# Optimization experiments

Measured on AMD Instinct MI355X. Metric: run time of the kernel, lower is better.

## Reference

```python
import jax, jax.numpy as jnp
import numpy as np

L, B, T, C, H, FF = 2, 2, 2048, 512, 8, 1024
HS = C // H  # head size
EPS = 1.1920929e-07  # torch float32 finfo eps (nn.RMSNorm default)


def setup_inputs() -> dict:
    key = jax.random.key(0)
    ks = jax.random.split(key, 20)
    s = 0.02
    return {
        "hidden": jax.random.normal(ks[0], (B, T, C), jnp.float32),
        "target": jax.random.normal(ks[1], (B, T, C), jnp.float32),
        # self-attn per-head projections (bias=False)
        "Wq_s": jax.random.normal(ks[2], (L, H, C, HS)) * s,
        "Wk_s": jax.random.normal(ks[3], (L, H, C, HS)) * s,
        "Wv_s": jax.random.normal(ks[4], (L, H, C, HS)) * s,
        "Wo_s": jax.random.normal(ks[5], (L, C, C)) * s,
        "bo_s": jnp.zeros((L, C)),
        # cross-attn per-head projections
        "Wq_x": jax.random.normal(ks[6], (L, H, C, HS)) * s,
        "Wk_x": jax.random.normal(ks[7], (L, H, C, HS)) * s,
        "Wv_x": jax.random.normal(ks[8], (L, H, C, HS)) * s,
        "Wo_x": jax.random.normal(ks[9], (L, C, C)) * s,
        "bo_x": jnp.zeros((L, C)),
        # FFN
        "W1": jax.random.normal(ks[10], (L, C, FF)) * s,
        "b1": jnp.zeros((L, FF)),
        "W2": jax.random.normal(ks[11], (L, FF, C)) * s,
        "b2": jnp.zeros((L, C)),
        # RMSNorm gains ln1..ln4
        "g1": jnp.ones((L, C)),
        "g2": jnp.ones((L, C)),
        "g3": jnp.ones((L, C)),
        "g4": jnp.ones((L, C)),
    }


def _rms(x, g):
    return x * jax.lax.rsqrt(jnp.mean(x * x, axis=-1, keepdims=True) + EPS) * g


def _attn(q_in, kv_in, Wq, Wk, Wv, Wo, bo, causal):
    # q_in: [B,Tq,C], kv_in: [B,Tk,C]; W*: [H,C,HS]
    q = jnp.einsum('btc,hcd->bhtd', q_in, Wq)
    k = jnp.einsum('bsc,hcd->bhsd', kv_in, Wk)
    v = jnp.einsum('bsc,hcd->bhsd', kv_in, Wv)
    wei = jnp.einsum('bhtd,bhsd->bhts', q, k) * (HS ** -0.5)  # [B,H,Tq,Tk]
    if causal:
        Tq, Tk = q_in.shape[1], kv_in.shape[1]
        mask = jnp.tril(jnp.ones((Tq, Tk), bool))
        wei = jnp.where(mask, wei, -jnp.inf)
    wei = jax.nn.softmax(wei, axis=-1)
    out = jnp.einsum('bhts,bhsd->bhtd', wei, v)
    out = out.transpose(0, 2, 1, 3).reshape(q_in.shape[0], q_in.shape[1], C)
    return out @ Wo + bo


def reference(hidden, target, Wq_s, Wk_s, Wv_s, Wo_s, bo_s,
              Wq_x, Wk_x, Wv_x, Wo_x, bo_x,
              W1, b1, W2, b2, g1, g2, g3, g4):
    t = target
    for l in range(L):
        # masked self-attention with RMSNorm pre-norm + residual
        t = t + _attn(_rms(t, g1[l]), _rms(t, g1[l]), Wq_s[l], Wk_s[l], Wv_s[l],
                      Wo_s[l], bo_s[l], causal=True)
        # cross-attention: K/V from ln2(hidden), Q from ln3(t)
        t = t + _attn(_rms(t, g3[l]), _rms(hidden, g2[l]), Wq_x[l], Wk_x[l], Wv_x[l],
                      Wo_x[l], bo_x[l], causal=False)
        # GELU FFN
        h = _rms(t, g4[l])
        t = t + (jax.nn.gelu(h @ W1[l] + b1[l], approximate=False) @ W2[l] + b2[l])
    return t
```

## Files before the change

kernel.cpp:

```cpp
#include <hip/hip_runtime.h>
#include <hip/hip_bf16.h>
#include <math.h>

#define L 2
#define B 2
#define T 2048
#define C 512
#define H 8
#define FF 1024
#define HS 64
#define EPSV 1.1920929e-07f

typedef __hip_bfloat16 bf16;
typedef __attribute__((ext_vector_type(8))) short short8;
typedef __attribute__((ext_vector_type(4))) float f32x4;

__device__ __forceinline__ float b2f(bf16 x) { return __bfloat162float(x); }

__device__ __forceinline__ void gl16(const unsigned short* g, unsigned short* l) {
    __builtin_amdgcn_global_load_lds(
        (const __attribute__((address_space(1))) unsigned int*)g,
        (__attribute__((address_space(3))) unsigned int*)l, 16, 0, 0);
}

__global__ void detect_k(const unsigned short* __restrict__ g1bits, int* __restrict__ flag) {
    if (threadIdx.x == 0 && blockIdx.x == 0)
        *flag = (g1bits[0] != (unsigned short)0x3F80u) ? 1 : 0;
}

__device__ __forceinline__ float ld_in(const void* p, size_t i, int fl) {
    return fl ? ((const float*)p)[i] : b2f(((const bf16*)p)[i]);
}

#define QKVT_TOT 1572864
#define WO_TOT 524288
#define W12_TOT 1048576
#define SM_TOT 9216
#define ACT_TOT 2097152
#define PREP_TOT (2 * QKVT_TOT + 2 * WO_TOT + 2 * W12_TOT + SM_TOT + 2 * ACT_TOT)

struct PrepArgs {
    const void *Wq_s, *Wk_s, *Wv_s, *Wo_s, *Wq_x, *Wk_x, *Wv_x, *Wo_x, *W1, *W2;
    const void* sm[8];
    const void *hidden, *target;
    bf16 *cQKVs, *cQKVx, *cWoTs, *cWoTx, *cW1T, *cW2T, *smallDst;
    float *hid, *t_buf;
    const int* flag;
};

__global__ void prep_k(PrepArgs pa) {
    long long i = (long long)blockIdx.x * 256 + threadIdx.x;
    if (i >= PREP_TOT) return;
    int fl = *pa.flag;
    if (i < 2LL * QKVT_TOT) {
        int which = i >= QKVT_TOT;
        int j = (int)(i - (long long)which * QKVT_TOT);
        int l = j / 786432, r = j - l * 786432;
        int n = r >> 9, c = r & 511;
        int p = n >> 9, nn = n & 511;
        int hh = nn >> 6, d = nn & 63;
        const void* src = which ? (p == 0 ? pa.Wq_x : p == 1 ? pa.Wk_x : pa.Wv_x)
                                : (p == 0 ? pa.Wq_s : p == 1 ? pa.Wk_s : pa.Wv_s);
        size_t si = ((size_t)(l * 8 + hh) * 512 + c) * 64 + d;
        (which ? pa.cQKVx : pa.cQKVs)[j] = __float2bfloat16(ld_in(src, si, fl));
        return;
    }
    i -= 2LL * QKVT_TOT;
    if (i < 2LL * WO_TOT) {
        int which = i >= WO_TOT;
        int j = (int)(i - (long long)which * WO_TOT);
        int l = j >> 18, r = j & 262143;
        int n = r >> 9, c = r & 511;
        size_t si = ((size_t)l << 18) + ((size_t)c << 9) + n;
        (which ? pa.cWoTx : pa.cWoTs)[j] = __float2bfloat16(ld_in(which ? pa.Wo_x : pa.Wo_s, si, fl));
        return;
    }
    i -= 2LL * WO_TOT;
    if (i < W12_TOT) {
        int j = (int)i;
        int l = j >> 19, r = j & 524287;
        int n = r >> 9, c = r & 511;
        size_t si = ((size_t)l << 19) + ((size_t)c << 10) + n;
        pa.cW1T[j] = __float2bfloat16(ld_in(pa.W1, si, fl));
        return;
    }
    i -= W12_TOT;
    if (i < W12_TOT) {
        int j = (int)i;
        int l = j >> 19, r = j & 524287;
        int n = r >> 10, c = r & 1023;
        size_t si = ((size_t)l << 19) + ((size_t)c << 9) + n;
        pa.cW2T[j] = __float2bfloat16(ld_in(pa.W2, si, fl));
        return;
    }
    i -= W12_TOT;
    if (i < SM_TOT) {
        int j = (int)i;
        const int cum[9] = {0, 1024, 2048, 4096, 5120, 6144, 7168, 8192, 9216};
        int k = 0;
        while (j >= cum[k + 1]) k++;
        pa.smallDst[j] = __float2bfloat16(ld_in(pa.sm[k], j - cum[k], fl));
        return;
    }
    i -= SM_TOT;
    if (i < ACT_TOT) {
        pa.hid[i] = ld_in(pa.hidden, (size_t)i, fl);
    } else {
        size_t j = i - ACT_TOT;
        pa.t_buf[j] = ld_in(pa.target, j, fl);
    }
}

__global__ void write_out_k(const float* __restrict__ in, void* __restrict__ out, int n,
                            const int* __restrict__ flag) {
    int i = blockIdx.x * blockDim.x + threadIdx.x;
    if (i >= n) return;
    if (*flag) ((float*)out)[i] = in[i];
    else       ((bf16*)out)[i] = __float2bfloat16(in[i]);
}

__global__ void rmsnorm_k(const float* __restrict__ x, const bf16* __restrict__ g,
                          bf16* __restrict__ y) {
    int row = blockIdx.x;
    int tid = threadIdx.x;
    const float* xr = x + (size_t)row * C;
    float v0 = xr[tid], v1 = xr[tid + 256];
    __shared__ float red[256];
    red[tid] = v0 * v0 + v1 * v1;
    __syncthreads();
    for (int s = 128; s > 0; s >>= 1) {
        if (tid < s) red[tid] += red[tid + s];
        __syncthreads();
    }
    float sc = rsqrtf(red[0] / (float)C + EPSV);
    y[(size_t)row * C + tid] = __float2bfloat16(v0 * sc * b2f(g[tid]));
    y[(size_t)row * C + tid + 256] = __float2bfloat16(v1 * sc * b2f(g[tid + 256]));
}

__global__ void rmsnorm2_k(const float* __restrict__ xa, const bf16* __restrict__ ga,
                           bf16* __restrict__ ya, const float* __restrict__ xb,
                           const bf16* __restrict__ gb, bf16* __restrict__ yb) {
    int sel = blockIdx.y;
    const float* x = sel ? xb : xa;
    const bf16* g = sel ? gb : ga;
    bf16* y = sel ? yb : ya;
    int row = blockIdx.x;
    int tid = threadIdx.x;
    const float* xr = x + (size_t)row * C;
    float v0 = xr[tid], v1 = xr[tid + 256];
    __shared__ float red[256];
    red[tid] = v0 * v0 + v1 * v1;
    __syncthreads();
    for (int s = 128; s > 0; s >>= 1) {
        if (tid < s) red[tid] += red[tid + s];
        __syncthreads();
    }
    float sc = rsqrtf(red[0] / (float)C + EPSV);
    y[(size_t)row * C + tid] = __float2bfloat16(v0 * sc * b2f(g[tid]));
    y[(size_t)row * C + tid + 256] = __float2bfloat16(v1 * sc * b2f(g[tid + 256]));
}

struct GDesc {
    const bf16* A; const bf16* Bt; const bf16* bias; float* resid; bf16* out;
    int N, K, ldOut, ep, nblkx, blkofs;
};
struct GBatch { GDesc d[3]; int nd; };

__global__ __launch_bounds__(256) void gemm64_k(GBatch gb) {
    int bid = blockIdx.x;
    int di = 0;
    if (gb.nd > 1 && bid >= gb.d[1].blkofs) di = 1;
    if (gb.nd > 2 && bid >= gb.d[2].blkofs) di = 2;
    GDesc g = gb.d[di];
    int lb = bid - g.blkofs;
    int bx = lb % g.nblkx, by = lb / g.nblkx;
    int m0 = by * 64, n0 = bx * 64;

    __shared__ alignas(16) unsigned short As[2][64 * 64];
    __shared__ alignas(16) unsigned short Bs[2][64 * 64];
    int tid = threadIdx.x, lane = tid & 63, wave = tid >> 6;
    int wr = wave >> 1, wc = wave & 1, quad = lane >> 4, l15 = lane & 15;
    const unsigned short* Au = (const unsigned short*)g.A;
    const unsigned short* Bu = (const unsigned short*)g.Bt;

    int r0 = tid >> 3, sg = tid & 7;
    int gs = sg ^ (r0 & 7);
    const unsigned short* agp0 = Au + (size_t)(m0 + r0) * g.K + gs * 8;
    const unsigned short* agp1 = Au + (size_t)(m0 + r0 + 32) * g.K + gs * 8;
    const unsigned short* bgp0 = Bu + (size_t)(n0 + r0) * g.K + gs * 8;
    const unsigned short* bgp1 = Bu + (size_t)(n0 + r0 + 32) * g.K + gs * 8;
    int wofs = wave * 512;

    f32x4 zf = {0.f, 0.f, 0.f, 0.f};
    f32x4 acc[2][2];
    acc[0][0] = zf; acc[0][1] = zf; acc[1][0] = zf; acc[1][1] = zf;

    int sws0 = ((quad) ^ (l15 & 7)) * 8;
    int sws1 = ((4 + quad) ^ (l15 & 7)) * 8;
    int arow = wr * 32 + l15, brow = wc * 32 + l15;

    int nk = g.K >> 6;
    {
        gl16(agp0, &As[0][wofs]);
        gl16(agp1, &As[0][wofs + 2048]);
        gl16(bgp0, &Bs[0][wofs]);
        gl16(bgp1, &Bs[0][wofs + 2048]);
    }
    __syncthreads();
    int buf = 0;
    for (int kt = 0; kt < nk; kt++) {
        if (kt + 1 < nk) {
            int ko = (kt + 1) << 6;
            gl16(agp0 + ko, &As[buf ^ 1][wofs]);
            gl16(agp1 + ko, &As[buf ^ 1][wofs + 2048]);
            gl16(bgp0 + ko, &Bs[buf ^ 1][wofs]);
            gl16(bgp1 + ko, &Bs[buf ^ 1][wofs + 2048]);
        }
        const unsigned short* Ab = As[buf];
        const unsigned short* Bb = Bs[buf];
        short8 a0[2], b0[2], a1[2], b1[2];
#pragma unroll
        for (int i = 0; i < 2; i++) {
            int ra = (arow + i * 16) << 6, rb = (brow + i * 16) << 6;
            a0[i] = *(const short8*)(Ab + ra + sws0);
            a1[i] = *(const short8*)(Ab + ra + sws1);
            b0[i] = *(const short8*)(Bb + rb + sws0);
            b1[i] = *(const short8*)(Bb + rb + sws1);
        }
#pragma unroll
        for (int mi = 0; mi < 2; mi++)
#pragma unroll
            for (int ni = 0; ni < 2; ni++) {
                acc[mi][ni] =
                    __builtin_amdgcn_mfma_f32_16x16x32_bf16(a0[mi], b0[ni], acc[mi][ni], 0, 0, 0);
                acc[mi][ni] =
                    __builtin_amdgcn_mfma_f32_16x16x32_bf16(a1[mi], b1[ni], acc[mi][ni], 0, 0, 0);
            }
        __syncthreads();
        buf ^= 1;
    }

#pragma unroll
    for (int mi = 0; mi < 2; mi++) {
#pragma unroll
        for (int ni = 0; ni < 2; ni++) {
            int colg = n0 + wc * 32 + ni * 16 + l15;
            float bv = (g.ep == 1 || g.ep == 2) ? b2f(g.bias[colg]) : 0.f;
#pragma unroll
            for (int r2 = 0; r2 < 4; r2++) {
                int rowg = m0 + wr * 32 + mi * 16 + quad * 4 + r2;
                float v = acc[mi][ni][r2];
                if (g.ep == 0) {
                    g.out[(size_t)rowg * g.ldOut + colg] = __float2bfloat16(v);
                } else if (g.ep == 1) {
                    g.resid[(size_t)rowg * g.ldOut + colg] += v + bv;
                } else if (g.ep == 2) {
                    float u = v + bv;
                    g.out[(size_t)rowg * g.ldOut + colg] =
                        __float2bfloat16(0.5f * u * (1.f + erff(u * 0.70710678118654752f)));
                } else {
                    g.out[((size_t)((colg >> 11) * 512 + rowg) << 11) + (colg & 2047)] =
                        __float2bfloat16(v);
                }
            }
        }
    }
}

#define PST 72
__global__ __launch_bounds__(256) void attn_mfma_k(const bf16* __restrict__ qkv,
                                                   const bf16* __restrict__ vT,
                                                   bf16* __restrict__ attnout, int causal) {
    __shared__ unsigned short KsA[2][4096], VtA[2][4096];
    __shared__ unsigned short Ps[4][16 * PST];
    int qt = causal ? (gridDim.x - 1 - blockIdx.x) : blockIdx.x;
    int h = blockIdx.y, b = blockIdx.z;
    int tid = threadIdx.x, lane = tid & 63, w = tid >> 6;
    int quad = lane >> 4, l15 = lane & 15;
    const unsigned short* qk = (const unsigned short*)qkv;
    const unsigned short* vTp = (const unsigned short*)vT + ((size_t)b * 512 + h * 64) * T;
    size_t rowbase = (size_t)b * T;
    int koff = 512 + h * 64;
    unsigned short* Pw = Ps[w];
    bf16* Pwb = (bf16*)Pw;

    const unsigned short* qrow = qk + (rowbase + qt * 64 + w * 16 + l15) * 1536 + h * 64;
    short8 aq0 = *(const short8*)(qrow + quad * 8);
    short8 aq1 = *(const short8*)(qrow + 32 + quad * 8);

    int srow = lane >> 3;
    int ssp = (lane & 7) ^ (srow & 7);

    f32x4 zf = {0.f, 0.f, 0.f, 0.f};
    f32x4 oacc[4];
#pragma unroll
    for (int i = 0; i < 4; i++) oacc[i] = zf;
    float lpart[4] = {0.f, 0.f, 0.f, 0.f};

    int nT = causal ? (qt + 1) : (T / 64);

#pragma unroll
    for (int j = 0; j < 2; j++) {
        int c = w * 2 + j;
        int r = c * 8 + srow;
        gl16(qk + (rowbase + r) * 1536 + koff + ssp * 8, KsA[0] + c * 512);
        gl16(vTp + (size_t)r * T + ssp * 8, VtA[0] + c * 512);
    }
    __syncthreads();

    int buf = 0;
    for (int st = 0; st < nT; st++) {
        if (st + 1 < nT) {
#pragma unroll
            for (int j = 0; j < 2; j++) {
                int c = w * 2 + j;
                int r = c * 8 + srow;
                gl16(qk + (rowbase + (st + 1) * 64 + r) * 1536 + koff + ssp * 8,
                     KsA[buf ^ 1] + c * 512);
                gl16(vTp + (size_t)r * T + (st + 1) * 64 + ssp * 8, VtA[buf ^ 1] + c * 512);
            }
        }

        const unsigned short* Kb = KsA[buf];
        const unsigned short* Vb = VtA[buf];

        f32x4 sacc[4];
#pragma unroll
        for (int i = 0; i < 4; i++) sacc[i] = zf;
#pragma unroll
        for (int ni = 0; ni < 4; ni++) {
            int rr = ni * 16 + l15;
            short8 bk0 = *(const short8*)(Kb + rr * 64 + ((quad ^ (rr & 7)) * 8));
            short8 bk1 = *(const short8*)(Kb + rr * 64 + (((4 + quad) ^ (rr & 7)) * 8));
            sacc[ni] = __builtin_amdgcn_mfma_f32_16x16x32_bf16(aq0, bk0, sacc[ni], 0, 0, 0);
            sacc[ni] = __builtin_amdgcn_mfma_f32_16x16x32_bf16(aq1, bk1, sacc[ni], 0, 0, 0);
        }

        bool diag = causal && (st == qt);
        int qrl = w * 16 + quad * 4;
#pragma unroll
        for (int reg = 0; reg < 4; reg++) {
            float lp = 0.f;
#pragma unroll
            for (int ni = 0; ni < 4; ni++) {
                int s_l = ni * 16 + l15;
                float p = __expf(sacc[ni][reg] * 0.125f);
                if (diag && s_l > qrl + reg) p = 0.f;
                lp += p;
                Pwb[(quad * 4 + reg) * PST + s_l] = __float2bfloat16(p);
            }
            lpart[reg] += lp;
        }

        short8 ap0 = *(const short8*)(Pw + l15 * PST + quad * 8);
        short8 ap1 = *(const short8*)(Pw + l15 * PST + 32 + quad * 8);
#pragma unroll
        for (int dj = 0; dj < 4; dj++) {
            int rr = dj * 16 + l15;
            short8 bv0 = *(const short8*)(Vb + rr * 64 + ((quad ^ (rr & 7)) * 8));
            short8 bv1 = *(const short8*)(Vb + rr * 64 + (((4 + quad) ^ (rr & 7)) * 8));
            oacc[dj] = __builtin_amdgcn_mfma_f32_16x16x32_bf16(ap0, bv0, oacc[dj], 0, 0, 0);
            oacc[dj] = __builtin_amdgcn_mfma_f32_16x16x32_bf16(ap1, bv1, oacc[dj], 0, 0, 0);
        }

        __syncthreads();
        buf ^= 1;
    }

#pragma unroll
    for (int reg = 0; reg < 4; reg++) {
#pragma unroll
        for (int mk = 1; mk < 16; mk <<= 1) lpart[reg] += __shfl_xor(lpart[reg], mk, 64);
        lpart[reg] = 1.0f / lpart[reg];
    }
#pragma unroll
    for (int dj = 0; dj < 4; dj++) {
        int d = dj * 16 + l15;
#pragma unroll
        for (int reg = 0; reg < 4; reg++) {
            int q = w * 16 + quad * 4 + reg;
            attnout[(rowbase + qt * 64 + q) * C + h * HS + d] =
                __float2bfloat16(oacc[dj][reg] * lpart[reg]);
        }
    }
}

extern "C" void kernel_launch(void* const* d_in, const int* in_sizes, int n_in,
                              void* d_out, int out_size, void* d_ws, size_t ws_size,
                              hipStream_t stream) {
    const int BTC = B * T * C;
    const int BTF = B * T * FF;

    char* wsb = (char*)d_ws;
    int* flag = (int*)wsb;
    bf16* cur = (bf16*)(wsb + 256);
    bf16* cQKVs = cur;   cur += QKVT_TOT;
    bf16* cQKVx = cur;   cur += QKVT_TOT;
    bf16* cWoTs = cur;   cur += WO_TOT;
    bf16* cWoTx = cur;   cur += WO_TOT;
    bf16* cW1T = cur;    cur += W12_TOT;
    bf16* cW2T = cur;    cur += W12_TOT;
    bf16* smallBase = cur;
    bf16* cbo_s = cur;   cur += L * C;
    bf16* cbo_x = cur;   cur += L * C;
    bf16* cb1 = cur;     cur += L * FF;
    bf16* cb2 = cur;     cur += L * C;
    bf16* cg1 = cur;     cur += L * C;
    bf16* cg2 = cur;     cur += L * C;
    bf16* cg3 = cur;     cur += L * C;
    bf16* cg4 = cur;     cur += L * C;
    bf16* n1 = cur;      cur += BTC;
    bf16* n2 = cur;      cur += BTC;
    bf16* qkvbuf = cur;  cur += B * T * 3 * C;
    bf16* vTbuf = cur;   cur += BTC;
    bf16* attnout = cur; cur += BTC;
    bf16* h1buf = cur;   cur += BTF;
    size_t f32_off = (((char*)cur - wsb) + 255) & ~(size_t)255;
    float* t_buf = (float*)(wsb + f32_off);
    float* hid = t_buf + BTC;

    dim3 blk256(256);
    detect_k<<<1, 64, 0, stream>>>((const unsigned short*)d_in[16], flag);

    PrepArgs pa;
    pa.Wq_s = d_in[2]; pa.Wk_s = d_in[3]; pa.Wv_s = d_in[4]; pa.Wo_s = d_in[5];
    pa.Wq_x = d_in[7]; pa.Wk_x = d_in[8]; pa.Wv_x = d_in[9]; pa.Wo_x = d_in[10];
    pa.W1 = d_in[12]; pa.W2 = d_in[14];
    pa.sm[0] = d_in[6];  pa.sm[1] = d_in[11]; pa.sm[2] = d_in[13]; pa.sm[3] = d_in[15];
    pa.sm[4] = d_in[16]; pa.sm[5] = d_in[17]; pa.sm[6] = d_in[18]; pa.sm[7] = d_in[19];
    pa.hidden = d_in[0]; pa.target = d_in[1];
    pa.cQKVs = cQKVs; pa.cQKVx = cQKVx; pa.cWoTs = cWoTs; pa.cWoTx = cWoTx;
    pa.cW1T = cW1T; pa.cW2T = cW2T; pa.smallDst = smallBase;
    pa.hid = hid; pa.t_buf = t_buf; pa.flag = flag;
    prep_k<<<(PREP_TOT + 255) / 256, blk256, 0, stream>>>(pa);

    const int M = B * T;
    dim3 attngrid(T / 64, H, B);

    for (int l = 0; l < L; l++) {
        bf16* qkvW_s = cQKVs + (size_t)l * 3 * C * C;
        bf16* qkvW_x = cQKVx + (size_t)l * 3 * C * C;
        bf16* woT_s = cWoTs + (size_t)l * C * C;
        bf16* woT_x = cWoTx + (size_t)l * C * C;
        bf16* w1T = cW1T + (size_t)l * C * FF;
        bf16* w2T = cW2T + (size_t)l * FF * C;

        rmsnorm_k<<<M, blk256, 0, stream>>>(t_buf, cg1 + l * C, n1);
        {
            GBatch gb;
            gb.nd = 2;
            gb.d[0] = {n1, qkvW_s, nullptr, nullptr, qkvbuf, 1024, C, 3 * C, 0, 16, 0};
            gb.d[1] = {qkvW_s + (size_t)1024 * C, n1, nullptr, nullptr, vTbuf,
                       M, C, 0, 3, 64, 1024};
            gemm64_k<<<1024 + 512, blk256, 0, stream>>>(gb);
        }
        attn_mfma_k<<<attngrid, blk256, 0, stream>>>(qkvbuf, vTbuf, attnout, 1);
        {
            GBatch gb;
            gb.nd = 1;
            gb.d[0] = {attnout, woT_s, cbo_s + l * C, t_buf, nullptr, C, C, C, 1, 8, 0};
            gemm64_k<<<512, blk256, 0, stream>>>(gb);
        }

        rmsnorm2_k<<<dim3(M, 2), blk256, 0, stream>>>(t_buf, cg3 + l * C, n1, hid, cg2 + l * C, n2);
        {
            GBatch gb;
            gb.nd = 3;
            gb.d[0] = {n1, qkvW_x, nullptr, nullptr, qkvbuf, C, C, 3 * C, 0, 8, 0};
            gb.d[1] = {n2, qkvW_x + (size_t)512 * C, nullptr, nullptr, qkvbuf + C,
                       C, C, 3 * C, 0, 8, 512};
            gb.d[2] = {qkvW_x + (size_t)1024 * C, n2, nullptr, nullptr, vTbuf,
                       M, C, 0, 3, 64, 1024};
            gemm64_k<<<512 + 512 + 512, blk256, 0, stream>>>(gb);
        }
        attn_mfma_k<<<attngrid, blk256, 0, stream>>>(qkvbuf, vTbuf, attnout, 0);
        {
            GBatch gb;
            gb.nd = 1;
            gb.d[0] = {attnout, woT_x, cbo_x + l * C, t_buf, nullptr, C, C, C, 1, 8, 0};
            gemm64_k<<<512, blk256, 0, stream>>>(gb);
        }

        rmsnorm_k<<<M, blk256, 0, stream>>>(t_buf, cg4 + l * C, n1);
        {
            GBatch gb;
            gb.nd = 1;
            gb.d[0] = {n1, w1T, cb1 + l * FF, nullptr, h1buf, FF, C, FF, 2, 16, 0};
            gemm64_k<<<1024, blk256, 0, stream>>>(gb);
        }
        {
            GBatch gb;
            gb.nd = 1;
            gb.d[0] = {h1buf, w2T, cb2 + l * C, t_buf, nullptr, C, FF, C, 1, 8, 0};
            gemm64_k<<<512, blk256, 0, stream>>>(gb);
        }
    }

    write_out_k<<<(BTC + 255) / 256, blk256, 0, stream>>>(t_buf, d_out, BTC, flag);
}
```

Before: 527.2 us.

## Tile weight transposes through shared memory, vectorize activation copy, load V directly

```diff
diff --git a/kernel.cpp b/kernel.cpp
--- a/kernel.cpp
+++ b/kernel.cpp
@@ -37,77 +37,95 @@
 #define W12_TOT 1048576
 #define SM_TOT 9216
 #define ACT_TOT 2097152
-#define PREP_TOT (2 * QKVT_TOT + 2 * WO_TOT + 2 * W12_TOT + SM_TOT + 2 * ACT_TOT)
-
-struct PrepArgs {
-    const void *Wq_s, *Wk_s, *Wv_s, *Wo_s, *Wq_x, *Wk_x, *Wv_x, *Wo_x, *W1, *W2;
+
+struct TrArgs {
+    const void *Wq_s, *Wk_s, *Wv_s, *Wq_x, *Wk_x, *Wv_x, *Wo_s, *Wo_x, *W1, *W2;
+    bf16 *cQKVs, *cQKVx, *cWoTs, *cWoTx, *cW1T, *cW2T;
+    const int* flag;
+};
+
+__global__ __launch_bounds__(256) void prep_tr_k(TrArgs a) {
+    __shared__ float tile[32][33];
+    int bid = blockIdx.x;
+    int fl = *a.flag;
+    const void* src; bf16* dst;
+    size_t sbase;
+    int srcLD, dstLD, r0, c0;
+    if (bid < 3072) {
+        int pid = bid >> 5, t = bid & 31;
+        int which = pid / 48, rem = pid % 48;
+        int l = rem / 24, rem2 = rem % 24;
+        int p = rem2 >> 3, hh = rem2 & 7;
+        src = which ? (p == 0 ? a.Wq_x : p == 1 ? a.Wk_x : a.Wv_x)
+                    : (p == 0 ? a.Wq_s : p == 1 ? a.Wk_s : a.Wv_s);
+        dst = (which ? a.cQKVx : a.cQKVs) + (size_t)l * 786432 + (size_t)(p * 512 + hh * 64) * 512;
+        sbase = (size_t)(l * 8 + hh) * 32768;
+        srcLD = 64; dstLD = 512;
+        r0 = (t >> 1) * 32; c0 = (t & 1) * 32;
+    } else if (bid < 4096) {
+        int b2 = bid - 3072, pid = b2 >> 8, t = b2 & 255;
+        int which = pid >> 1, l = pid & 1;
+        src = which ? a.Wo_x : a.Wo_s;
+        dst = (which ? a.cWoTx : a.cWoTs) + (size_t)l * 262144;
+        sbase = (size_t)l * 262144;
+        srcLD = 512; dstLD = 512;
+        r0 = (t >> 4) * 32; c0 = (t & 15) * 32;
+    } else if (bid < 5120) {
+        int b2 = bid - 4096, l = b2 >> 9, t = b2 & 511;
+        src = a.W1; dst = a.cW1T + (size_t)l * 524288; sbase = (size_t)l * 524288;
+        srcLD = 1024; dstLD = 512;
+        r0 = (t >> 5) * 32; c0 = (t & 31) * 32;
+    } else {
+        int b2 = bid - 5120, l = b2 >> 9, t = b2 & 511;
+        src = a.W2; dst = a.cW2T + (size_t)l * 524288; sbase = (size_t)l * 524288;
+        srcLD = 512; dstLD = 1024;
+        r0 = (t >> 4) * 32; c0 = (t & 15) * 32;
+    }
+    int tx = threadIdx.x & 31, ty = threadIdx.x >> 5;
+#pragma unroll
+    for (int i = 0; i < 4; i++)
+        tile[ty + i * 8][tx] = ld_in(src, sbase + (size_t)(r0 + ty + i * 8) * srcLD + c0 + tx, fl);
+    __syncthreads();
+#pragma unroll
+    for (int i = 0; i < 4; i++)
+        dst[(size_t)(c0 + ty + i * 8) * dstLD + r0 + tx] = __float2bfloat16(tile[tx][ty + i * 8]);
+}
+
+#define ACTQ 1048576
+struct SmArgs {
     const void* sm[8];
     const void *hidden, *target;
-    bf16 *cQKVs, *cQKVx, *cWoTs, *cWoTx, *cW1T, *cW2T, *smallDst;
+    bf16* smallDst;
     float *hid, *t_buf;
     const int* flag;
 };
 
-__global__ void prep_k(PrepArgs pa) {
-    long long i = (long long)blockIdx.x * 256 + threadIdx.x;
-    if (i >= PREP_TOT) return;
-    int fl = *pa.flag;
-    if (i < 2LL * QKVT_TOT) {
-        int which = i >= QKVT_TOT;
-        int j = (int)(i - (long long)which * QKVT_TOT);
-        int l = j / 786432, r = j - l * 786432;
-        int n = r >> 9, c = r & 511;
-        int p = n >> 9, nn = n & 511;
-        int hh = nn >> 6, d = nn & 63;
-        const void* src = which ? (p == 0 ? pa.Wq_x : p == 1 ? pa.Wk_x : pa.Wv_x)
-                                : (p == 0 ? pa.Wq_s : p == 1 ? pa.Wk_s : pa.Wv_s);
-        size_t si = ((size_t)(l * 8 + hh) * 512 + c) * 64 + d;
-        (which ? pa.cQKVx : pa.cQKVs)[j] = __float2bfloat16(ld_in(src, si, fl));
-        return;
-    }
-    i -= 2LL * QKVT_TOT;
-    if (i < 2LL * WO_TOT) {
-        int which = i >= WO_TOT;
-        int j = (int)(i - (long long)which * WO_TOT);
-        int l = j >> 18, r = j & 262143;
-        int n = r >> 9, c = r & 511;
-        size_t si = ((size_t)l << 18) + ((size_t)c << 9) + n;
-        (which ? pa.cWoTx : pa.cWoTs)[j] = __float2bfloat16(ld_in(which ? pa.Wo_x : pa.Wo_s, si, fl));
-        return;
-    }
-    i -= 2LL * WO_TOT;
-    if (i < W12_TOT) {
-        int j = (int)i;
-        int l = j >> 19, r = j & 524287;
-        int n = r >> 9, c = r & 511;
-        size_t si = ((size_t)l << 19) + ((size_t)c << 10) + n;
-        pa.cW1T[j] = __float2bfloat16(ld_in(pa.W1, si, fl));
-        return;
-    }
-    i -= W12_TOT;
-    if (i < W12_TOT) {
-        int j = (int)i;
-        int l = j >> 19, r = j & 524287;
-        int n = r >> 10, c = r & 1023;
-        size_t si = ((size_t)l << 19) + ((size_t)c << 9) + n;
-        pa.cW2T[j] = __float2bfloat16(ld_in(pa.W2, si, fl));
-        return;
-    }
-    i -= W12_TOT;
+__global__ void prep_small_k(SmArgs s) {
+    int i = blockIdx.x * 256 + threadIdx.x;
+    int fl = *s.flag;
     if (i < SM_TOT) {
-        int j = (int)i;
         const int cum[9] = {0, 1024, 2048, 4096, 5120, 6144, 7168, 8192, 9216};
         int k = 0;
-        while (j >= cum[k + 1]) k++;
-        pa.smallDst[j] = __float2bfloat16(ld_in(pa.sm[k], j - cum[k], fl));
+        while (i >= cum[k + 1]) k++;
+        s.smallDst[i] = __float2bfloat16(ld_in(s.sm[k], i - cum[k], fl));
         return;
     }
-    i -= SM_TOT;
-    if (i < ACT_TOT) {
-        pa.hid[i] = ld_in(pa.hidden, (size_t)i, fl);
+    int q = i - SM_TOT;
+    if (q >= ACTQ) return;
+    int half = q >= (ACTQ / 2);
+    size_t e = (size_t)(q - half * (ACTQ / 2)) * 4;
+    const void* src = half ? s.target : s.hidden;
+    float* dstf = half ? s.t_buf : s.hid;
+    if (fl) {
+        *(float4*)(dstf + e) = *(const float4*)((const float*)src + e);
     } else {
-        size_t j = i - ACT_TOT;
-        pa.t_buf[j] = ld_in(pa.target, j, fl);
+        ushort4 u = *(const ushort4*)((const unsigned short*)src + e);
+        float4 v;
+        v.x = __uint_as_float((unsigned)u.x << 16);
+        v.y = __uint_as_float((unsigned)u.y << 16);
+        v.z = __uint_as_float((unsigned)u.z << 16);
+        v.w = __uint_as_float((unsigned)u.w << 16);
+        *(float4*)(dstf + e) = v;
     }
 }
 
@@ -271,7 +289,7 @@
 __global__ __launch_bounds__(256) void attn_mfma_k(const bf16* __restrict__ qkv,
                                                    const bf16* __restrict__ vT,
                                                    bf16* __restrict__ attnout, int causal) {
-    __shared__ unsigned short KsA[2][4096], VtA[2][4096];
+    __shared__ alignas(16) unsigned short KsA[2][4096];
     __shared__ unsigned short Ps[4][16 * PST];
     int qt = causal ? (gridDim.x - 1 - blockIdx.x) : blockIdx.x;
     int h = blockIdx.y, b = blockIdx.z;
@@ -304,7 +322,6 @@
         int c = w * 2 + j;
         int r = c * 8 + srow;
         gl16(qk + (rowbase + r) * 1536 + koff + ssp * 8, KsA[0] + c * 512);
-        gl16(vTp + (size_t)r * T + ssp * 8, VtA[0] + c * 512);
     }
     __syncthreads();
 
@@ -317,12 +334,10 @@
                 int r = c * 8 + srow;
                 gl16(qk + (rowbase + (st + 1) * 64 + r) * 1536 + koff + ssp * 8,
                      KsA[buf ^ 1] + c * 512);
-                gl16(vTp + (size_t)r * T + (st + 1) * 64 + ssp * 8, VtA[buf ^ 1] + c * 512);
             }
         }
 
         const unsigned short* Kb = KsA[buf];
-        const unsigned short* Vb = VtA[buf];
 
         f32x4 sacc[4];
 #pragma unroll
@@ -334,6 +349,14 @@
             short8 bk1 = *(const short8*)(Kb + rr * 64 + (((4 + quad) ^ (rr & 7)) * 8));
             sacc[ni] = __builtin_amdgcn_mfma_f32_16x16x32_bf16(aq0, bk0, sacc[ni], 0, 0, 0);
             sacc[ni] = __builtin_amdgcn_mfma_f32_16x16x32_bf16(aq1, bk1, sacc[ni], 0, 0, 0);
+        }
+
+        short8 bv0[4], bv1[4];
+#pragma unroll
+        for (int dj = 0; dj < 4; dj++) {
+            const unsigned short* vrow = vTp + (size_t)(dj * 16 + l15) * T + st * 64 + quad * 8;
+            bv0[dj] = *(const short8*)(vrow);
+            bv1[dj] = *(const short8*)(vrow + 32);
         }
 
         bool diag = causal && (st == qt);
@@ -356,11 +379,8 @@
         short8 ap1 = *(const short8*)(Pw + l15 * PST + 32 + quad * 8);
 #pragma unroll
         for (int dj = 0; dj < 4; dj++) {
-            int rr = dj * 16 + l15;
-            short8 bv0 = *(const short8*)(Vb + rr * 64 + ((quad ^ (rr & 7)) * 8));
-            short8 bv1 = *(const short8*)(Vb + rr * 64 + (((4 + quad) ^ (rr & 7)) * 8));
-            oacc[dj] = __builtin_amdgcn_mfma_f32_16x16x32_bf16(ap0, bv0, oacc[dj], 0, 0, 0);
-            oacc[dj] = __builtin_amdgcn_mfma_f32_16x16x32_bf16(ap1, bv1, oacc[dj], 0, 0, 0);
+            oacc[dj] = __builtin_amdgcn_mfma_f32_16x16x32_bf16(ap0, bv0[dj], oacc[dj], 0, 0, 0);
+            oacc[dj] = __builtin_amdgcn_mfma_f32_16x16x32_bf16(ap1, bv1[dj], oacc[dj], 0, 0, 0);
         }
 
         __syncthreads();
@@ -422,17 +442,20 @@
     dim3 blk256(256);
     detect_k<<<1, 64, 0, stream>>>((const unsigned short*)d_in[16], flag);
 
-    PrepArgs pa;
-    pa.Wq_s = d_in[2]; pa.Wk_s = d_in[3]; pa.Wv_s = d_in[4]; pa.Wo_s = d_in[5];
-    pa.Wq_x = d_in[7]; pa.Wk_x = d_in[8]; pa.Wv_x = d_in[9]; pa.Wo_x = d_in[10];
-    pa.W1 = d_in[12]; pa.W2 = d_in[14];
-    pa.sm[0] = d_in[6];  pa.sm[1] = d_in[11]; pa.sm[2] = d_in[13]; pa.sm[3] = d_in[15];
-    pa.sm[4] = d_in[16]; pa.sm[5] = d_in[17]; pa.sm[6] = d_in[18]; pa.sm[7] = d_in[19];
-    pa.hidden = d_in[0]; pa.target = d_in[1];
-    pa.cQKVs = cQKVs; pa.cQKVx = cQKVx; pa.cWoTs = cWoTs; pa.cWoTx = cWoTx;
-    pa.cW1T = cW1T; pa.cW2T = cW2T; pa.smallDst = smallBase;
-    pa.hid = hid; pa.t_buf = t_buf; pa.flag = flag;
-    prep_k<<<(PREP_TOT + 255) / 256, blk256, 0, stream>>>(pa);
+    TrArgs ta;
+    ta.Wq_s = d_in[2]; ta.Wk_s = d_in[3]; ta.Wv_s = d_in[4];
+    ta.Wq_x = d_in[7]; ta.Wk_x = d_in[8]; ta.Wv_x = d_in[9];
+    ta.Wo_s = d_in[5]; ta.Wo_x = d_in[10]; ta.W1 = d_in[12]; ta.W2 = d_in[14];
+    ta.cQKVs = cQKVs; ta.cQKVx = cQKVx; ta.cWoTs = cWoTs; ta.cWoTx = cWoTx;
+    ta.cW1T = cW1T; ta.cW2T = cW2T; ta.flag = flag;
+    prep_tr_k<<<6144, blk256, 0, stream>>>(ta);
+
+    SmArgs sa;
+    sa.sm[0] = d_in[6];  sa.sm[1] = d_in[11]; sa.sm[2] = d_in[13]; sa.sm[3] = d_in[15];
+    sa.sm[4] = d_in[16]; sa.sm[5] = d_in[17]; sa.sm[6] = d_in[18]; sa.sm[7] = d_in[19];
+    sa.hidden = d_in[0]; sa.target = d_in[1];
+    sa.smallDst = smallBase; sa.hid = hid; sa.t_buf = t_buf; sa.flag = flag;
+    prep_small_k<<<(SM_TOT + ACTQ + 255) / 256, blk256, 0, stream>>>(sa);
 
     const int M = B * T;
     dim3 attngrid(T / 64, H, B);
```

Result: slower. 655.3 us (+24.3%).
